# Kernel tuning notes

Hardware: AMD Instinct MI355X
Metric: run time of the kernel (lower is better)

## Reference

```python
import jax, jax.numpy as jnp
import numpy as np

B, N, SEQ_LEN, OUT_LEN, E = 4, 5000, 128, 128, 80000
C_IN = SEQ_LEN + OUT_LEN  # DConv input is concat([X, H])


def setup_inputs() -> dict:
    key = jax.random.key(0)
    ks = jax.random.split(key, 9)
    scale = 0.02
    return {
        "x": jax.random.normal(ks[0], (B, N, SEQ_LEN), dtype=jnp.float32),
        "edge_index": jax.random.randint(ks[1], (2, E), 0, N, dtype=jnp.int32),
        "edge_weight": jax.random.uniform(ks[2], (E,), dtype=jnp.float32),
        "Wz": scale * jax.random.normal(ks[3], (2, 2, C_IN, OUT_LEN), dtype=jnp.float32),
        "bz": jnp.zeros((OUT_LEN,), jnp.float32),
        "Wr": scale * jax.random.normal(ks[4], (2, 2, C_IN, OUT_LEN), dtype=jnp.float32),
        "br": jnp.zeros((OUT_LEN,), jnp.float32),
        "Wh": scale * jax.random.normal(ks[5], (2, 2, C_IN, OUT_LEN), dtype=jnp.float32),
        "bh": jnp.zeros((OUT_LEN,), jnp.float32),
    }


def reference(x, edge_index, edge_weight, Wz, bz, Wr, br, Wh, bh):
    src, dst = edge_index[0], edge_index[1]
    # weighted out-/in-degrees and random-walk normalization (safe reciprocal)
    deg_out = jax.ops.segment_sum(edge_weight, src, num_segments=N)
    deg_in = jax.ops.segment_sum(edge_weight, dst, num_segments=N)
    dinv_out = jnp.where(deg_out > 0, 1.0 / deg_out, 0.0)
    dinv_in = jnp.where(deg_in > 0, 1.0 / deg_in, 0.0)
    coef_o = edge_weight * dinv_out[src]  # D_out^-1 W, per-edge
    coef_i = edge_weight * dinv_in[dst]   # D_in^-1 W^T, per-edge

    def dconv(Xc, W, b):
        # K=2 diffusion conv: identity terms + 1-hop forward + 1-hop reverse
        H = Xc @ (W[0, 0] + W[1, 0])
        Tx_o = jax.ops.segment_sum(coef_o[:, None] * Xc[src], dst, num_segments=N)
        Tx_i = jax.ops.segment_sum(coef_i[:, None] * Xc[dst], src, num_segments=N)
        return H + Tx_o @ W[0, 1] + Tx_i @ W[1, 1] + b

    def cell(X):  # X: [N, SEQ_LEN]; hidden state starts at zero each call
        H0 = jnp.zeros((N, OUT_LEN), X.dtype)
        Xc = jnp.concatenate([X, H0], axis=-1)
        Z = jax.nn.sigmoid(dconv(Xc, Wz, bz))
        R = jax.nn.sigmoid(dconv(Xc, Wr, br))
        Xc2 = jnp.concatenate([X, H0 * R], axis=-1)
        H_tilde = jnp.tanh(dconv(Xc2, Wh, bh))
        return Z * H0 + (1.0 - Z) * H_tilde

    return jax.vmap(cell)(x)  # [B, N, OUT_LEN]
```

## Files before the change

### kernel.cpp

```cpp
#include <hip/hip_runtime.h>
#include <math.h>

#define NN   5000
#define BB   4
#define SEQ  128
#define OUTC 128
#define EE   80000
#define KTOT 384
#define CTOT 256
#define MTOT (BB * NN)
#define MPAD 20096
#define CAP  64
#define EBLK 313

typedef __attribute__((ext_vector_type(8))) short bf16x8;
typedef __attribute__((ext_vector_type(4))) float f32x4;

__device__ inline unsigned short f2bf(float f) {
    union { float f; unsigned u; } a; a.f = f;
    unsigned r = a.u + 0x7FFF + ((a.u >> 16) & 1);
    return (unsigned short)(r >> 16);
}

__global__ __launch_bounds__(256) void k_zero(float* __restrict__ z) {
    int i = blockIdx.x * blockDim.x + threadIdx.x;
    if (i < 5000) {
        f32x4 zz = {0.f, 0.f, 0.f, 0.f};
        *(f32x4*)&z[i * 4] = zz;
    }
}

__global__ __launch_bounds__(256) void k_bucket_fold(
        const int* __restrict__ ei, const float* __restrict__ ew,
        const float* __restrict__ Wz, const float* __restrict__ bz,
        const float* __restrict__ Wh, const float* __restrict__ bh,
        float* deg_out, float* deg_in,
        unsigned* cnt_in, unsigned* cnt_out,
        int2* __restrict__ bin, int2* __restrict__ bout,
        unsigned short* __restrict__ WT, float* __restrict__ bcat2) {
    int bid = blockIdx.x;
    if (bid < EBLK) {
        int e = bid * 256 + threadIdx.x;
        if (e >= EE) return;
        int s = ei[e], d = ei[EE + e];
        float w = ew[e];
        atomicAdd(&deg_out[s], w);
        atomicAdd(&deg_in[d], w);
        unsigned p = atomicAdd(&cnt_in[d], 1u);
        if (p < CAP) bin[((size_t)d << 6) + p] = make_int2(s, __float_as_int(w));
        unsigned q = atomicAdd(&cnt_out[s], 1u);
        if (q < CAP) bout[((size_t)s << 6) + q] = make_int2(d, __float_as_int(w));
    } else {
        int i = (bid - EBLK) * 256 + threadIdx.x;
        if (i < CTOT) bcat2[i] = (i & 1) ? bh[i >> 1] : bz[i >> 1];
        int cc = i / KTOT, k = i % KTOT;
        int gate = cc & 1, o = cc >> 1;
        const float* W = gate ? Wh : Wz;
        float v;
        if (k < 128)      v = W[(size_t)k * 128 + o] + W[(size_t)(512 + k) * 128 + o];
        else if (k < 256) v = W[(size_t)(256 + (k - 128)) * 128 + o];
        else              v = W[(size_t)(768 + (k - 256)) * 128 + o];
        WT[(size_t)cc * KTOT + k] = f2bf(v);
    }
}

__global__ __launch_bounds__(256) void k_diffuse(
        const float* __restrict__ x,
        const float* __restrict__ deg_out, const float* __restrict__ deg_in,
        const unsigned* __restrict__ cnt_in, const unsigned* __restrict__ cnt_out,
        const int2* __restrict__ bin, const int2* __restrict__ bout,
        unsigned short* __restrict__ Inb) {
    __shared__ int2 sbA[4][CAP + 2], sbB[4][CAP + 2];
    int bid = blockIdx.x;
    int slot = bid & 7, pos = bid >> 3;
    int b = slot >> 1;
    int wv = threadIdx.x >> 6;
    int n = (pos * 2 + (slot & 1)) * 4 + wv;
    int l = threadIdx.x & 63;
    int h = l >> 5, q = l & 31;
    const float* xb = x + (size_t)b * NN * SEQ;

    f32x4 xo = *(const f32x4*)&xb[(size_t)n * SEQ + 4 * q];

    int mi = (int)min(cnt_in[n], (unsigned)CAP);
    int mo = (int)min(cnt_out[n], (unsigned)CAP);
    if (l < mi) {
        int2 e = bin[((size_t)n << 6) + l];
        float dg = deg_out[e.x];
        float cf = dg > 0.f ? __int_as_float(e.y) / dg : 0.f;
        sbA[wv][l] = make_int2(e.x, __float_as_int(cf));
    } else if (l == mi) {
        sbA[wv][l] = make_int2(0, 0);
    }
    if (l < mo) {
        int2 e = bout[((size_t)n << 6) + l];
        float dg = deg_in[e.x];
        float cf = dg > 0.f ? __int_as_float(e.y) / dg : 0.f;
        sbB[wv][l] = make_int2(e.x, __float_as_int(cf));
    } else if (l == mo) {
        sbB[wv][l] = make_int2(0, 0);
    }
    int mie = (mi + 1) & ~1, moe = (mo + 1) & ~1;

    f32x4 ao = {0.f, 0.f, 0.f, 0.f}, ai = {0.f, 0.f, 0.f, 0.f};
    int j = 0;
    for (; j + 3 < mie; j += 4) {
        int2 e0 = sbA[wv][j + h], e1 = sbA[wv][j + 2 + h];
        f32x4 v0 = *(const f32x4*)&xb[(size_t)e0.x * SEQ + 4 * q];
        f32x4 v1 = *(const f32x4*)&xb[(size_t)e1.x * SEQ + 4 * q];
        float c0 = __int_as_float(e0.y), c1 = __int_as_float(e1.y);
        ao.x += c0 * v0.x; ao.y += c0 * v0.y; ao.z += c0 * v0.z; ao.w += c0 * v0.w;
        ao.x += c1 * v1.x; ao.y += c1 * v1.y; ao.z += c1 * v1.z; ao.w += c1 * v1.w;
    }
    for (; j < mie; j += 2) {
        int2 e0 = sbA[wv][j + h];
        f32x4 v0 = *(const f32x4*)&xb[(size_t)e0.x * SEQ + 4 * q];
        float c0 = __int_as_float(e0.y);
        ao.x += c0 * v0.x; ao.y += c0 * v0.y; ao.z += c0 * v0.z; ao.w += c0 * v0.w;
    }
    j = 0;
    for (; j + 3 < moe; j += 4) {
        int2 e0 = sbB[wv][j + h], e1 = sbB[wv][j + 2 + h];
        f32x4 v0 = *(const f32x4*)&xb[(size_t)e0.x * SEQ + 4 * q];
        f32x4 v1 = *(const f32x4*)&xb[(size_t)e1.x * SEQ + 4 * q];
        float c0 = __int_as_float(e0.y), c1 = __int_as_float(e1.y);
        ai.x += c0 * v0.x; ai.y += c0 * v0.y; ai.z += c0 * v0.z; ai.w += c0 * v0.w;
        ai.x += c1 * v1.x; ai.y += c1 * v1.y; ai.z += c1 * v1.z; ai.w += c1 * v1.w;
    }
    for (; j < moe; j += 2) {
        int2 e0 = sbB[wv][j + h];
        f32x4 v0 = *(const f32x4*)&xb[(size_t)e0.x * SEQ + 4 * q];
        float c0 = __int_as_float(e0.y);
        ai.x += c0 * v0.x; ai.y += c0 * v0.y; ai.z += c0 * v0.z; ai.w += c0 * v0.w;
    }

    ao.x += __shfl_xor(ao.x, 32); ao.y += __shfl_xor(ao.y, 32);
    ao.z += __shfl_xor(ao.z, 32); ao.w += __shfl_xor(ao.w, 32);
    ai.x += __shfl_xor(ai.x, 32); ai.y += __shfl_xor(ai.y, 32);
    ai.z += __shfl_xor(ai.z, 32); ai.w += __shfl_xor(ai.w, 32);

    unsigned short* r = Inb + (size_t)(b * NN + n) * KTOT;
    f32x4 av = h ? ai : ao;
    uint2 pk;
    pk.x = (unsigned)f2bf(av.x) | ((unsigned)f2bf(av.y) << 16);
    pk.y = (unsigned)f2bf(av.z) | ((unsigned)f2bf(av.w) << 16);
    *(uint2*)&r[(h ? 256 : 128) + 4 * q] = pk;
    if (!h) {
        uint2 px;
        px.x = (unsigned)f2bf(xo.x) | ((unsigned)f2bf(xo.y) << 16);
        px.y = (unsigned)f2bf(xo.z) | ((unsigned)f2bf(xo.w) << 16);
        *(uint2*)&r[4 * q] = px;
    }
}

__global__ __launch_bounds__(256) void k_mm(
        const unsigned short* __restrict__ Inb, const unsigned short* __restrict__ WT,
        const float* __restrict__ bcat2, float* __restrict__ out) {
    __shared__ unsigned short lA[2][4096];
    __shared__ unsigned short lB[2][4096];
    int t = threadIdx.x, w = t >> 6, l = t & 63;
    int lr = l & 15, lk = l >> 4;
    int n0 = blockIdx.x * 128;
    int c0 = blockIdx.y * 128;
    int wr = w >> 1, wc = w & 1;
    f32x4 acc[4][4] = {};

#define STAGE(buf, k0)                                                            \
    {                                                                             \
        _Pragma("unroll")                                                         \
        for (int qq = 0; qq < 2; ++qq) {                                          \
            int f = w * 2 + qq;                                                   \
            const unsigned short* sa = Inb + (size_t)(n0 + f * 16 + lr) * KTOT + (k0) + lk * 8; \
            __builtin_amdgcn_global_load_lds(                                     \
                (const __attribute__((address_space(1))) void*)sa,                \
                (__attribute__((address_space(3))) void*)&lA[buf][f * 512], 16, 0, 0); \
            const unsigned short* sb = WT + (size_t)(c0 + f * 16 + lr) * KTOT + (k0) + lk * 8; \
            __builtin_amdgcn_global_load_lds(                                     \
                (const __attribute__((address_space(1))) void*)sb,                \
                (__attribute__((address_space(3))) void*)&lB[buf][f * 512], 16, 0, 0); \
        }                                                                         \
    }

    STAGE(0, 0);
    asm volatile("s_waitcnt vmcnt(0)" ::: "memory");
    __builtin_amdgcn_s_barrier();

    int cur = 0;
#pragma unroll
    for (int ks = 0; ks < 12; ++ks) {
        if (ks < 11) STAGE(cur ^ 1, (ks + 1) * 32);
        bf16x8 a[4], bfr[4];
#pragma unroll
        for (int i = 0; i < 4; ++i) a[i] = *(const bf16x8*)&lA[cur][(wr * 4 + i) * 512 + l * 8];
#pragma unroll
        for (int jj = 0; jj < 4; ++jj) bfr[jj] = *(const bf16x8*)&lB[cur][(wc * 4 + jj) * 512 + l * 8];
#pragma unroll
        for (int i = 0; i < 4; ++i)
#pragma unroll
            for (int jj = 0; jj < 4; ++jj)
                acc[i][jj] = __builtin_amdgcn_mfma_f32_16x16x32_bf16(a[i], bfr[jj], acc[i][jj], 0, 0, 0);
        asm volatile("s_waitcnt vmcnt(0)" ::: "memory");
        __builtin_amdgcn_s_barrier();
        cur ^= 1;
    }
#undef STAGE

    int row_base = n0 + wr * 64;
    bool odd = (l & 1);
#pragma unroll
    for (int jj = 0; jj < 4; ++jj) {
        int cc = c0 + wc * 64 + jj * 16 + lr;
        float bias = bcat2[cc];
        int o = cc >> 1;
#pragma unroll
        for (int i = 0; i < 4; ++i) {
#pragma unroll
            for (int rr = 0; rr < 4; ++rr) {
                float v = acc[i][jj][rr] + bias;
                float ex = __expf(odd ? 2.f * v : v);
                float u = odd ? (1.f - 2.f / (ex + 1.f)) : (1.f / (1.f + ex));
                float g = __shfl_xor(u, 1);
                if (!odd) {
                    int row = row_base + i * 16 + lk * 4 + rr;
                    if (row < MTOT) out[(size_t)row * OUTC + o] = u * g;
                }
            }
        }
    }
}

extern "C" void kernel_launch(void* const* d_in, const int* in_sizes, int n_in,
                              void* d_out, int out_size, void* d_ws, size_t ws_size,
                              hipStream_t stream) {
    const float* x  = (const float*)d_in[0];
    const int*   ei = (const int*)d_in[1];
    const float* ew = (const float*)d_in[2];
    const float* Wz = (const float*)d_in[3];
    const float* bz = (const float*)d_in[4];
    const float* Wh = (const float*)d_in[7];
    const float* bh = (const float*)d_in[8];

    float* ws = (float*)d_ws;
    float*    deg_out = ws + 0;
    float*    deg_in  = ws + 5000;
    unsigned* cnt_in  = (unsigned*)(ws + 10000);
    unsigned* cnt_out = (unsigned*)(ws + 15000);
    float*    bcat2   = ws + 20000;
    unsigned short* WT = (unsigned short*)(ws + 20256);
    int2*     bin  = (int2*)(ws + 69408);
    int2*     bout = (int2*)(ws + 709408);
    unsigned short* Inb = (unsigned short*)(ws + 1349408);

    k_zero<<<20, 256, 0, stream>>>(ws);
    k_bucket_fold<<<EBLK + CTOT * KTOT / 256, 256, 0, stream>>>(
        ei, ew, Wz, bz, Wh, bh, deg_out, deg_in, cnt_in, cnt_out, bin, bout, WT, bcat2);
    k_diffuse<<<NN, 256, 0, stream>>>(x, deg_out, deg_in, cnt_in, cnt_out, bin, bout, Inb);
    dim3 g(MPAD / 128, 2);
    k_mm<<<g, 256, 0, stream>>>(Inb, WT, bcat2, (float*)d_out);
}
```

Before: 77.79 us.

## Gather bf16 copy of x in diffusion and triple-buffer GEMM LDS stages

```diff
diff --git a/kernel.cpp b/kernel.cpp
--- a/kernel.cpp
+++ b/kernel.cpp
@@ -12,6 +12,8 @@
 #define MPAD 20096
 #define CAP  64
 #define EBLK 313
+#define FBLK 384
+#define XBLK 1250
 
 typedef __attribute__((ext_vector_type(8))) short bf16x8;
 typedef __attribute__((ext_vector_type(4))) float f32x4;
@@ -32,12 +34,14 @@
 
 __global__ __launch_bounds__(256) void k_bucket_fold(
         const int* __restrict__ ei, const float* __restrict__ ew,
+        const float* __restrict__ x,
         const float* __restrict__ Wz, const float* __restrict__ bz,
         const float* __restrict__ Wh, const float* __restrict__ bh,
         float* deg_out, float* deg_in,
         unsigned* cnt_in, unsigned* cnt_out,
         int2* __restrict__ bin, int2* __restrict__ bout,
-        unsigned short* __restrict__ WT, float* __restrict__ bcat2) {
+        unsigned short* __restrict__ WT, float* __restrict__ bcat2,
+        unsigned short* __restrict__ xb16) {
     int bid = blockIdx.x;
     if (bid < EBLK) {
         int e = bid * 256 + threadIdx.x;
@@ -50,7 +54,7 @@
         if (p < CAP) bin[((size_t)d << 6) + p] = make_int2(s, __float_as_int(w));
         unsigned q = atomicAdd(&cnt_out[s], 1u);
         if (q < CAP) bout[((size_t)s << 6) + q] = make_int2(d, __float_as_int(w));
-    } else {
+    } else if (bid < EBLK + FBLK) {
         int i = (bid - EBLK) * 256 + threadIdx.x;
         if (i < CTOT) bcat2[i] = (i & 1) ? bh[i >> 1] : bz[i >> 1];
         int cc = i / KTOT, k = i % KTOT;
@@ -61,26 +65,46 @@
         else if (k < 256) v = W[(size_t)(256 + (k - 128)) * 128 + o];
         else              v = W[(size_t)(768 + (k - 256)) * 128 + o];
         WT[(size_t)cc * KTOT + k] = f2bf(v);
-    }
-}
+    } else {
+        int j = (bid - EBLK - FBLK) * 256 + threadIdx.x;
+        if (j < (BB * NN * SEQ) / 8) {
+            const float4* xp = (const float4*)x;
+            float4 v0 = xp[(size_t)j * 2], v1 = xp[(size_t)j * 2 + 1];
+            uint4 pk;
+            pk.x = (unsigned)f2bf(v0.x) | ((unsigned)f2bf(v0.y) << 16);
+            pk.y = (unsigned)f2bf(v0.z) | ((unsigned)f2bf(v0.w) << 16);
+            pk.z = (unsigned)f2bf(v1.x) | ((unsigned)f2bf(v1.y) << 16);
+            pk.w = (unsigned)f2bf(v1.z) | ((unsigned)f2bf(v1.w) << 16);
+            ((uint4*)xb16)[j] = pk;
+        }
+    }
+}
+
+#define ACC8(A, v, cf) {                                              \
+    A[0] += (cf) * __uint_as_float((v).x << 16);                      \
+    A[1] += (cf) * __uint_as_float((v).x & 0xFFFF0000u);              \
+    A[2] += (cf) * __uint_as_float((v).y << 16);                      \
+    A[3] += (cf) * __uint_as_float((v).y & 0xFFFF0000u);              \
+    A[4] += (cf) * __uint_as_float((v).z << 16);                      \
+    A[5] += (cf) * __uint_as_float((v).z & 0xFFFF0000u);              \
+    A[6] += (cf) * __uint_as_float((v).w << 16);                      \
+    A[7] += (cf) * __uint_as_float((v).w & 0xFFFF0000u); }
 
 __global__ __launch_bounds__(256) void k_diffuse(
-        const float* __restrict__ x,
+        const unsigned short* __restrict__ xb16,
         const float* __restrict__ deg_out, const float* __restrict__ deg_in,
         const unsigned* __restrict__ cnt_in, const unsigned* __restrict__ cnt_out,
         const int2* __restrict__ bin, const int2* __restrict__ bout,
         unsigned short* __restrict__ Inb) {
-    __shared__ int2 sbA[4][CAP + 2], sbB[4][CAP + 2];
+    __shared__ int2 sbA[4][CAP + 4], sbB[4][CAP + 4];
     int bid = blockIdx.x;
     int slot = bid & 7, pos = bid >> 3;
     int b = slot >> 1;
     int wv = threadIdx.x >> 6;
     int n = (pos * 2 + (slot & 1)) * 4 + wv;
     int l = threadIdx.x & 63;
-    int h = l >> 5, q = l & 31;
-    const float* xb = x + (size_t)b * NN * SEQ;
-
-    f32x4 xo = *(const f32x4*)&xb[(size_t)n * SEQ + 4 * q];
+    int h = l >> 4, q = l & 15;
+    const unsigned short* xb = xb16 + (size_t)b * NN * SEQ;
 
     int mi = (int)min(cnt_in[n], (unsigned)CAP);
     int mo = (int)min(cnt_out[n], (unsigned)CAP);
@@ -89,7 +113,7 @@
         float dg = deg_out[e.x];
         float cf = dg > 0.f ? __int_as_float(e.y) / dg : 0.f;
         sbA[wv][l] = make_int2(e.x, __float_as_int(cf));
-    } else if (l == mi) {
+    } else if (l < ((mi + 3) & ~3)) {
         sbA[wv][l] = make_int2(0, 0);
     }
     if (l < mo) {
@@ -97,67 +121,76 @@
         float dg = deg_in[e.x];
         float cf = dg > 0.f ? __int_as_float(e.y) / dg : 0.f;
         sbB[wv][l] = make_int2(e.x, __float_as_int(cf));
-    } else if (l == mo) {
+    } else if (l < ((mo + 3) & ~3)) {
         sbB[wv][l] = make_int2(0, 0);
     }
-    int mie = (mi + 1) & ~1, moe = (mo + 1) & ~1;
-
-    f32x4 ao = {0.f, 0.f, 0.f, 0.f}, ai = {0.f, 0.f, 0.f, 0.f};
+    int mie = (mi + 3) & ~3, moe = (mo + 3) & ~3;
+
+    float ao[8] = {0.f, 0.f, 0.f, 0.f, 0.f, 0.f, 0.f, 0.f};
+    float ai[8] = {0.f, 0.f, 0.f, 0.f, 0.f, 0.f, 0.f, 0.f};
     int j = 0;
-    for (; j + 3 < mie; j += 4) {
-        int2 e0 = sbA[wv][j + h], e1 = sbA[wv][j + 2 + h];
-        f32x4 v0 = *(const f32x4*)&xb[(size_t)e0.x * SEQ + 4 * q];
-        f32x4 v1 = *(const f32x4*)&xb[(size_t)e1.x * SEQ + 4 * q];
+    for (; j + 7 < mie; j += 8) {
+        int2 e0 = sbA[wv][j + h], e1 = sbA[wv][j + 4 + h];
+        uint4 v0 = *(const uint4*)&xb[(size_t)e0.x * SEQ + 8 * q];
+        uint4 v1 = *(const uint4*)&xb[(size_t)e1.x * SEQ + 8 * q];
         float c0 = __int_as_float(e0.y), c1 = __int_as_float(e1.y);
-        ao.x += c0 * v0.x; ao.y += c0 * v0.y; ao.z += c0 * v0.z; ao.w += c0 * v0.w;
-        ao.x += c1 * v1.x; ao.y += c1 * v1.y; ao.z += c1 * v1.z; ao.w += c1 * v1.w;
-    }
-    for (; j < mie; j += 2) {
+        ACC8(ao, v0, c0);
+        ACC8(ao, v1, c1);
+    }
+    for (; j < mie; j += 4) {
         int2 e0 = sbA[wv][j + h];
-        f32x4 v0 = *(const f32x4*)&xb[(size_t)e0.x * SEQ + 4 * q];
+        uint4 v0 = *(const uint4*)&xb[(size_t)e0.x * SEQ + 8 * q];
         float c0 = __int_as_float(e0.y);
-        ao.x += c0 * v0.x; ao.y += c0 * v0.y; ao.z += c0 * v0.z; ao.w += c0 * v0.w;
+        ACC8(ao, v0, c0);
     }
     j = 0;
-    for (; j + 3 < moe; j += 4) {
-        int2 e0 = sbB[wv][j + h], e1 = sbB[wv][j + 2 + h];
-        f32x4 v0 = *(const f32x4*)&xb[(size_t)e0.x * SEQ + 4 * q];
-        f32x4 v1 = *(const f32x4*)&xb[(size_t)e1.x * SEQ + 4 * q];
+    for (; j + 7 < moe; j += 8) {
+        int2 e0 = sbB[wv][j + h], e1 = sbB[wv][j + 4 + h];
+        uint4 v0 = *(const uint4*)&xb[(size_t)e0.x * SEQ + 8 * q];
+        uint4 v1 = *(const uint4*)&xb[(size_t)e1.x * SEQ + 8 * q];
         float c0 = __int_as_float(e0.y), c1 = __int_as_float(e1.y);
-        ai.x += c0 * v0.x; ai.y += c0 * v0.y; ai.z += c0 * v0.z; ai.w += c0 * v0.w;
-        ai.x += c1 * v1.x; ai.y += c1 * v1.y; ai.z += c1 * v1.z; ai.w += c1 * v1.w;
-    }
-    for (; j < moe; j += 2) {
+        ACC8(ai, v0, c0);
+        ACC8(ai, v1, c1);
+    }
+    for (; j < moe; j += 4) {
         int2 e0 = sbB[wv][j + h];
-        f32x4 v0 = *(const f32x4*)&xb[(size_t)e0.x * SEQ + 4 * q];
+        uint4 v0 = *(const uint4*)&xb[(size_t)e0.x * SEQ + 8 * q];
         float c0 = __int_as_float(e0.y);
-        ai.x += c0 * v0.x; ai.y += c0 * v0.y; ai.z += c0 * v0.z; ai.w += c0 * v0.w;
-    }
-
-    ao.x += __shfl_xor(ao.x, 32); ao.y += __shfl_xor(ao.y, 32);
-    ao.z += __shfl_xor(ao.z, 32); ao.w += __shfl_xor(ao.w, 32);
-    ai.x += __shfl_xor(ai.x, 32); ai.y += __shfl_xor(ai.y, 32);
-    ai.z += __shfl_xor(ai.z, 32); ai.w += __shfl_xor(ai.w, 32);
-
-    unsigned short* r = Inb + (size_t)(b * NN + n) * KTOT;
-    f32x4 av = h ? ai : ao;
-    uint2 pk;
-    pk.x = (unsigned)f2bf(av.x) | ((unsigned)f2bf(av.y) << 16);
-    pk.y = (unsigned)f2bf(av.z) | ((unsigned)f2bf(av.w) << 16);
-    *(uint2*)&r[(h ? 256 : 128) + 4 * q] = pk;
-    if (!h) {
-        uint2 px;
-        px.x = (unsigned)f2bf(xo.x) | ((unsigned)f2bf(xo.y) << 16);
-        px.y = (unsigned)f2bf(xo.z) | ((unsigned)f2bf(xo.w) << 16);
-        *(uint2*)&r[4 * q] = px;
+        ACC8(ai, v0, c0);
+    }
+
+#pragma unroll
+    for (int r = 0; r < 8; ++r) {
+        ao[r] += __shfl_xor(ao[r], 16); ao[r] += __shfl_xor(ao[r], 32);
+        ai[r] += __shfl_xor(ai[r], 16); ai[r] += __shfl_xor(ai[r], 32);
+    }
+
+    unsigned short* rw = Inb + (size_t)(b * NN + n) * KTOT;
+    if (h == 0) {
+        uint4 pk;
+        pk.x = (unsigned)f2bf(ao[0]) | ((unsigned)f2bf(ao[1]) << 16);
+        pk.y = (unsigned)f2bf(ao[2]) | ((unsigned)f2bf(ao[3]) << 16);
+        pk.z = (unsigned)f2bf(ao[4]) | ((unsigned)f2bf(ao[5]) << 16);
+        pk.w = (unsigned)f2bf(ao[6]) | ((unsigned)f2bf(ao[7]) << 16);
+        *(uint4*)&rw[128 + 8 * q] = pk;
+    } else if (h == 1) {
+        uint4 pk;
+        pk.x = (unsigned)f2bf(ai[0]) | ((unsigned)f2bf(ai[1]) << 16);
+        pk.y = (unsigned)f2bf(ai[2]) | ((unsigned)f2bf(ai[3]) << 16);
+        pk.z = (unsigned)f2bf(ai[4]) | ((unsigned)f2bf(ai[5]) << 16);
+        pk.w = (unsigned)f2bf(ai[6]) | ((unsigned)f2bf(ai[7]) << 16);
+        *(uint4*)&rw[256 + 8 * q] = pk;
+    } else if (h == 2) {
+        uint4 xv = *(const uint4*)&xb[(size_t)n * SEQ + 8 * q];
+        *(uint4*)&rw[8 * q] = xv;
     }
 }
 
 __global__ __launch_bounds__(256) void k_mm(
         const unsigned short* __restrict__ Inb, const unsigned short* __restrict__ WT,
         const float* __restrict__ bcat2, float* __restrict__ out) {
-    __shared__ unsigned short lA[2][4096];
-    __shared__ unsigned short lB[2][4096];
+    __shared__ unsigned short lA[3][4096];
+    __shared__ unsigned short lB[3][4096];
     int t = threadIdx.x, w = t >> 6, l = t & 63;
     int lr = l & 15, lk = l >> 4;
     int n0 = blockIdx.x * 128;
@@ -182,26 +215,25 @@
     }
 
     STAGE(0, 0);
-    asm volatile("s_waitcnt vmcnt(0)" ::: "memory");
-    __builtin_amdgcn_s_barrier();
-
-    int cur = 0;
+    STAGE(1, 32);
+
 #pragma unroll
     for (int ks = 0; ks < 12; ++ks) {
-        if (ks < 11) STAGE(cur ^ 1, (ks + 1) * 32);
+        if (ks < 11) asm volatile("s_waitcnt vmcnt(4)" ::: "memory");
+        else         asm volatile("s_waitcnt vmcnt(0)" ::: "memory");
+        __builtin_amdgcn_s_barrier();
+        const int bf = ks % 3;
         bf16x8 a[4], bfr[4];
 #pragma unroll
-        for (int i = 0; i < 4; ++i) a[i] = *(const bf16x8*)&lA[cur][(wr * 4 + i) * 512 + l * 8];
-#pragma unroll
-        for (int jj = 0; jj < 4; ++jj) bfr[jj] = *(const bf16x8*)&lB[cur][(wc * 4 + jj) * 512 + l * 8];
+        for (int i = 0; i < 4; ++i) a[i] = *(const bf16x8*)&lA[bf][(wr * 4 + i) * 512 + l * 8];
+#pragma unroll
+        for (int jj = 0; jj < 4; ++jj) bfr[jj] = *(const bf16x8*)&lB[bf][(wc * 4 + jj) * 512 + l * 8];
 #pragma unroll
         for (int i = 0; i < 4; ++i)
 #pragma unroll
             for (int jj = 0; jj < 4; ++jj)
                 acc[i][jj] = __builtin_amdgcn_mfma_f32_16x16x32_bf16(a[i], bfr[jj], acc[i][jj], 0, 0, 0);
-        asm volatile("s_waitcnt vmcnt(0)" ::: "memory");
-        __builtin_amdgcn_s_barrier();
-        cur ^= 1;
+        if (ks + 2 < 12) STAGE((ks + 2) % 3, (ks + 2) * 32);
     }
 #undef STAGE
 
@@ -249,12 +281,15 @@
     unsigned short* WT = (unsigned short*)(ws + 20256);
     int2*     bin  = (int2*)(ws + 69408);
     int2*     bout = (int2*)(ws + 709408);
-    unsigned short* Inb = (unsigned short*)(ws + 1349408);
+    unsigned short* xb16 = (unsigned short*)(ws + 1349408);
+    unsigned short* Inb = (unsigned short*)(ws + 2629408);
 
     k_zero<<<20, 256, 0, stream>>>(ws);
-    k_bucket_fold<<<EBLK + CTOT * KTOT / 256, 256, 0, stream>>>(
-        ei, ew, Wz, bz, Wh, bh, deg_out, deg_in, cnt_in, cnt_out, bin, bout, WT, bcat2);
-    k_diffuse<<<NN, 256, 0, stream>>>(x, deg_out, deg_in, cnt_in, cnt_out, bin, bout, Inb);
+    k_bucket_fold<<<EBLK + FBLK + XBLK, 256, 0, stream>>>(
+        ei, ew, x, Wz, bz, Wh, bh, deg_out, deg_in, cnt_in, cnt_out,
+        bin, bout, WT, bcat2, xb16);
+    k_diffuse<<<NN, 256, 0, stream>>>(xb16, deg_out, deg_in, cnt_in, cnt_out,
+                                      bin, bout, Inb);
     dim3 g(MPAD / 128, 2);
     k_mm<<<g, 256, 0, stream>>>(Inb, WT, bcat2, (float*)d_out);
 }
```

After: 75.19 us. 3.3% less time.
